# Kernel tuning notes

Hardware: AMD Instinct MI355X
Metric: run time of the kernel (lower is better)

Reference implementation:

```python
import jax, jax.numpy as jnp
import numpy as np

TOP_K = 2  # num_experts_per_token


def setup_inputs() -> dict:
    key = jax.random.key(0)
    k1, k2, k3, k4 = jax.random.split(key, 4)
    B, S, D, F, E = 2, 2048, 1024, 4096, 8
    hidden_states = jax.random.normal(k1, (B, S, D), dtype=jnp.float32)
    # router: nn.Linear(D, E, bias=False) -> weight [E, D]
    Wr = jax.random.normal(k2, (E, D), dtype=jnp.float32) * (1.0 / np.sqrt(D))
    # expert FFNs: W1 [E, D, F] (first Linear, transposed), W2 [E, F, D]
    W1 = jax.random.normal(k3, (E, D, F), dtype=jnp.float32) * (1.0 / np.sqrt(D))
    W2 = jax.random.normal(k4, (E, F, D), dtype=jnp.float32) * (1.0 / np.sqrt(F))
    return {"hidden_states": hidden_states, "Wr": Wr, "W1": W1, "W2": W2}


def reference(hidden_states, Wr, W1, W2):
    B, S, D = hidden_states.shape
    E = Wr.shape[0]
    x = hidden_states.reshape(-1, D)                      # [T, D]
    T = x.shape[0]

    router_logits = x @ Wr.T                              # [T, E]
    routing_weights = jax.nn.softmax(router_logits, axis=-1)
    top_w, top_idx = jax.lax.top_k(routing_weights, TOP_K)  # [T, K]
    top_w = top_w / jnp.sum(top_w, axis=-1, keepdims=True)

    # combine weights scattered into dense [T, E] (zero for unselected experts)
    comb = jnp.zeros((T, E), dtype=x.dtype).at[
        jnp.arange(T)[:, None], top_idx
    ].add(top_w)

    # per-expert FFN: SiLU(x @ W1) @ W2, computed densely then masked-combined
    h = jax.nn.silu(jnp.einsum('td,edf->tef', x, W1))     # [T, E, F]
    y = jnp.einsum('tef,efd->ted', h, W2)                 # [T, E, D]
    out = jnp.einsum('te,ted->td', comb, y)               # [T, D]
    return out.reshape(B, S, D)
```

## Files before the change

### kernel.cpp

```cpp
#include <hip/hip_runtime.h>
#include <hip/hip_bf16.h>

#define T_TOK 4096
#define DDIM  1024
#define FDIM  4096
#define NEXP  8
#define TLMAX 136

typedef __attribute__((ext_vector_type(8))) short bf16x8;
typedef __attribute__((ext_vector_type(4))) float f32x4;

__device__ __forceinline__ void gl2lds16(const void* g, void* l) {
  __builtin_amdgcn_global_load_lds((const __attribute__((address_space(1))) void*)g,
                                   (__attribute__((address_space(3))) void*)l,
                                   16, 0, 0);
}

__device__ __forceinline__ unsigned short f2bf(float f) {
  unsigned u = __float_as_uint(f);
  unsigned r = (u + 0x7fffu + ((u >> 16) & 1u)) >> 16;
  return (unsigned short)r;
}
__device__ __forceinline__ float bf2f(unsigned short u) {
  return __uint_as_float((unsigned)u << 16);
}

__global__ __launch_bounds__(256) void moe_router(
    const float* __restrict__ x, const float* __restrict__ Wr,
    unsigned short* __restrict__ xb, int* __restrict__ te, float* __restrict__ tw) {
  __shared__ float wr[NEXP * DDIM];
  const int tid = threadIdx.x;
#pragma unroll
  for (int i = 0; i < NEXP * DDIM / 256; ++i) wr[i * 256 + tid] = Wr[i * 256 + tid];
  __syncthreads();

  const int wave = tid >> 6, lane = tid & 63;
  const int t = blockIdx.x * 4 + wave;
  const float* xr = x + (size_t)t * DDIM;
  const int d0 = lane * 16;

  float4 xv[4];
#pragma unroll
  for (int j = 0; j < 4; ++j) xv[j] = *(const float4*)(xr + d0 + j * 4);

  float lg[NEXP];
#pragma unroll
  for (int e = 0; e < NEXP; ++e) {
    float s = 0.f;
#pragma unroll
    for (int j = 0; j < 4; ++j) {
      float4 wv = *(const float4*)(&wr[e * DDIM + d0 + j * 4]);
      s += xv[j].x * wv.x + xv[j].y * wv.y + xv[j].z * wv.z + xv[j].w * wv.w;
    }
    lg[e] = s;
  }
#pragma unroll
  for (int e = 0; e < NEXP; ++e) {
#pragma unroll
    for (int off = 32; off > 0; off >>= 1) lg[e] += __shfl_xor(lg[e], off);
  }

#pragma unroll
  for (int j = 0; j < 4; ++j) {
    ushort4 o;
    o.x = f2bf(xv[j].x); o.y = f2bf(xv[j].y); o.z = f2bf(xv[j].z); o.w = f2bf(xv[j].w);
    *(ushort4*)(xb + (size_t)t * DDIM + d0 + j * 4) = o;
  }

  if (lane == 0) {
    int i0 = 0;
#pragma unroll
    for (int e = 1; e < NEXP; ++e) if (lg[e] > lg[i0]) i0 = e;
    int i1 = (i0 == 0) ? 1 : 0;
#pragma unroll
    for (int e = 0; e < NEXP; ++e) if (e != i0 && lg[e] > lg[i1]) i1 = e;
    float w0 = 1.f / (1.f + __expf(lg[i1] - lg[i0]));
    te[t * 2 + 0] = i0; te[t * 2 + 1] = i1;
    tw[t * 2 + 0] = w0; tw[t * 2 + 1] = 1.f - w0;
  }
}

__global__ __launch_bounds__(256) void moe_count(const int* __restrict__ te,
                                                 int* __restrict__ counts) {
  __shared__ int lh[NEXP];
  const int tid = threadIdx.x;
  if (tid < NEXP) lh[tid] = 0;
  __syncthreads();
  const int t = blockIdx.x * 256 + tid;
  atomicAdd(&lh[te[t * 2 + 0]], 1);
  atomicAdd(&lh[te[t * 2 + 1]], 1);
  __syncthreads();
  if (tid < NEXP) atomicAdd(&counts[tid], lh[tid]);
}

__global__ void moe_prefix(const int* __restrict__ counts, int* __restrict__ offs,
                           int* __restrict__ fill, int* __restrict__ tcnt,
                           int* __restrict__ tlist) {
  if (threadIdx.x == 0) {
    int s = 0, tt = 0;
    for (int e = 0; e < NEXP; ++e) {
      offs[e] = s;
      int c = counts[e];
      s += c;
      fill[e] = 0;
      for (int mt = 0; mt * 64 < c; ++mt) tlist[tt++] = (e << 8) | mt;
    }
    offs[NEXP] = s;
    tcnt[0] = tt;
  }
}

__global__ __launch_bounds__(256) void moe_scatter(
    const int* __restrict__ te, const int* __restrict__ offs, int* __restrict__ fill,
    int* __restrict__ rows, int* __restrict__ slot) {
  __shared__ int lcnt[NEXP], lbase[NEXP];
  const int tid = threadIdx.x;
  if (tid < NEXP) lcnt[tid] = 0;
  __syncthreads();
  const int t = blockIdx.x * 256 + tid;
  const int e0 = te[t * 2 + 0], e1 = te[t * 2 + 1];
  const int r0 = atomicAdd(&lcnt[e0], 1);
  const int r1 = atomicAdd(&lcnt[e1], 1);
  __syncthreads();
  if (tid < NEXP) lbase[tid] = atomicAdd(&fill[tid], lcnt[tid]);
  __syncthreads();
  int p0 = offs[e0] + lbase[e0] + r0;
  int p1 = offs[e1] + lbase[e1] + r1;
  rows[p0] = t; rows[p1] = t;
  slot[t * 2 + 0] = p0; slot[t * 2 + 1] = p1;
}

__global__ __launch_bounds__(256) void wconv_t(const float* __restrict__ W,
                                               unsigned short* __restrict__ Wt,
                                               int K, int N) {
  __shared__ unsigned short t[64][65];
  const int e = blockIdx.z;
  const float* src = W + (size_t)e * K * N + (size_t)(blockIdx.y * 64) * N + blockIdx.x * 64;
  unsigned short* dst = Wt + (size_t)e * N * K + (size_t)(blockIdx.x * 64) * K + blockIdx.y * 64;
  const int tid = threadIdx.x;
  const int rr = tid >> 4;
  const int cc4 = (tid & 15) * 4;
#pragma unroll
  for (int i = 0; i < 4; ++i) {
    int r = i * 16 + rr;
    float4 v = *(const float4*)(src + (size_t)r * N + cc4);
    t[cc4 + 0][r] = f2bf(v.x);
    t[cc4 + 1][r] = f2bf(v.y);
    t[cc4 + 2][r] = f2bf(v.z);
    t[cc4 + 3][r] = f2bf(v.w);
  }
  __syncthreads();
  const int k8 = (tid & 7) * 8;
#pragma unroll
  for (int i = 0; i < 2; ++i) {
    int c = i * 32 + (tid >> 3);
    uint4 pk;
    pk.x = (unsigned)t[c][k8 + 0] | ((unsigned)t[c][k8 + 1] << 16);
    pk.y = (unsigned)t[c][k8 + 2] | ((unsigned)t[c][k8 + 3] << 16);
    pk.z = (unsigned)t[c][k8 + 4] | ((unsigned)t[c][k8 + 5] << 16);
    pk.w = (unsigned)t[c][k8 + 6] | ((unsigned)t[c][k8 + 7] << 16);
    *(uint4*)(dst + (size_t)c * K + k8) = pk;
  }
}

template <int KD, int KSLICE, int ND, bool GATHER, bool DOSILU>
__global__ __launch_bounds__(512, 4) void moe_gemm(
    const unsigned short* __restrict__ Asrc, const unsigned short* __restrict__ Wt,
    const int* __restrict__ rows, const int* __restrict__ offs,
    const int* __restrict__ tcnt, const int* __restrict__ tlist,
    unsigned short* __restrict__ Out) {
  constexpr int BM = 64, BN = 256;
  constexpr int S = KD / KSLICE;
  constexpr int NTN = ND / BN;
  constexpr int NPAN = NTN * S;
  constexpr int NB = TLMAX * NPAN;
  constexpr int CB = BN / 64;
  constexpr int MF = BM / 32, NF = 4;

  __shared__ alignas(16) unsigned short Alds[2][BM * 64];
  __shared__ alignas(16) unsigned short Blds[2][BN * 64];

  const int bid = blockIdx.x;
  const int orig = (bid & 7) * (NB >> 3) + (bid >> 3);
  const int TT = tcnt[0];
  if (orig >= TT * NPAN) return;
  const int tt = orig % TT;
  const int panel = orig / TT;
  const int nt = panel % NTN;
  const int ksl = panel / NTN;
  const int pk = tlist[tt];
  const int e = pk >> 8, mt = pk & 255;

  const int base = offs[e];
  const int cnt = offs[e + 1] - base;
  const int m0 = mt * BM;
  const int valid = min(BM, cnt - m0);
  const size_t koff = (size_t)ksl * KSLICE;

  const int tid = threadIdx.x;
  const int w = tid >> 6, lane = tid & 63;
  const int wm = w >> 2, wn = w & 3;

  const int n0 = nt * BN;
  const unsigned short* Wb = Wt + (size_t)e * ND * KD + (size_t)n0 * KD + koff;

  const int cc8 = ((lane & 7) ^ (lane >> 3)) * 8;
  const int ar = w * 8 + (lane >> 3);
  const int aslot = base + m0 + min(ar, valid - 1);
  const size_t aoff = (size_t)(GATHER ? rows[aslot] : aslot) * KD + koff + cc8;
  size_t boff[CB];
#pragma unroll
  for (int s = 0; s < CB; ++s) {
    int r = s * 64 + w * 8 + (lane >> 3);
    boff[s] = (size_t)r * KD + cc8;
  }

  f32x4 acc[MF][NF] = {};

#define STAGE(b, k0)                                                         \
  {                                                                          \
    gl2lds16(Asrc + aoff + (k0), &Alds[b][w * 512]);                         \
    _Pragma("unroll") for (int s = 0; s < CB; ++s)                           \
        gl2lds16(Wb + boff[s] + (k0), &Blds[b][(s * 512 + w * 64) * 8]);     \
  }

#define COMPUTE(b)                                                           \
  {                                                                          \
    _Pragma("unroll") for (int ks = 0; ks < 2; ++ks) {                       \
      bf16x8 af[MF], bfr[NF];                                                \
      _Pragma("unroll") for (int mf = 0; mf < MF; ++mf) {                    \
        int row = wm * 32 + mf * 16 + (lane & 15);                           \
        int cc = ks * 4 + (lane >> 4);                                       \
        af[mf] = *(const bf16x8*)((const char*)&Alds[b][0] + row * 128 +     \
                                  ((cc ^ (row & 7)) * 16));                  \
      }                                                                      \
      _Pragma("unroll") for (int nf = 0; nf < NF; ++nf) {                    \
        int col = wn * 64 + nf * 16 + (lane & 15);                           \
        int cc = ks * 4 + (lane >> 4);                                       \
        bfr[nf] = *(const bf16x8*)((const char*)&Blds[b][0] + col * 128 +    \
                                   ((cc ^ (col & 7)) * 16));                 \
      }                                                                      \
      _Pragma("unroll") for (int mf = 0; mf < MF; ++mf)                      \
          _Pragma("unroll") for (int nf = 0; nf < NF; ++nf)                  \
              acc[mf][nf] = __builtin_amdgcn_mfma_f32_16x16x32_bf16(         \
                  af[mf], bfr[nf], acc[mf][nf], 0, 0, 0);                    \
    }                                                                        \
  }

  constexpr int NK = KSLICE / 64;
  STAGE(0, 0);
  for (int t = 0; t < NK; t += 2) {
    STAGE(1, (t + 1) * 64);
    asm volatile("s_waitcnt vmcnt(5)" ::: "memory");
    __builtin_amdgcn_s_barrier();
    COMPUTE(0);
    __builtin_amdgcn_s_barrier();
    if (t + 2 < NK) {
      STAGE(0, (t + 2) * 64);
      asm volatile("s_waitcnt vmcnt(5)" ::: "memory");
    } else {
      asm volatile("s_waitcnt vmcnt(0)" ::: "memory");
    }
    __builtin_amdgcn_s_barrier();
    COMPUTE(1);
    __builtin_amdgcn_s_barrier();
  }
#undef STAGE
#undef COMPUTE

  unsigned short* Op = Out + (size_t)ksl * 8192 * ND;
  const int q = lane >> 4, c16 = lane & 15;
#pragma unroll
  for (int mf = 0; mf < MF; ++mf) {
#pragma unroll
    for (int r = 0; r < 4; ++r) {
      int lrow = wm * 32 + mf * 16 + q * 4 + r;
      if (lrow < valid) {
#pragma unroll
        for (int nf = 0; nf < NF; ++nf) {
          int gcol = n0 + wn * 64 + nf * 16 + c16;
          float v = acc[mf][nf][r];
          if (DOSILU) v = v / (1.f + __expf(-v));
          Op[(size_t)(base + m0 + lrow) * ND + gcol] = f2bf(v);
        }
      }
    }
  }
}

__global__ __launch_bounds__(256) void moe_combine(
    const unsigned short* __restrict__ y, const int* __restrict__ slot,
    const float* __restrict__ tw, float* __restrict__ out) {
  const int t = blockIdx.x;
  const int s0 = slot[t * 2], s1 = slot[t * 2 + 1];
  const float w0 = tw[t * 2], w1 = tw[t * 2 + 1];
  const int i = threadIdx.x * 4;
  ushort4 a = *(const ushort4*)(y + (size_t)s0 * DDIM + i);
  ushort4 b = *(const ushort4*)(y + (size_t)(8192 + s0) * DDIM + i);
  ushort4 c = *(const ushort4*)(y + (size_t)s1 * DDIM + i);
  ushort4 d = *(const ushort4*)(y + (size_t)(8192 + s1) * DDIM + i);
  float4 r;
  r.x = w0 * (bf2f(a.x) + bf2f(b.x)) + w1 * (bf2f(c.x) + bf2f(d.x));
  r.y = w0 * (bf2f(a.y) + bf2f(b.y)) + w1 * (bf2f(c.y) + bf2f(d.y));
  r.z = w0 * (bf2f(a.z) + bf2f(b.z)) + w1 * (bf2f(c.z) + bf2f(d.z));
  r.w = w0 * (bf2f(a.w) + bf2f(b.w)) + w1 * (bf2f(c.w) + bf2f(d.w));
  *(float4*)(out + (size_t)t * DDIM + i) = r;
}

extern "C" void kernel_launch(void* const* d_in, const int* in_sizes, int n_in,
                              void* d_out, int out_size, void* d_ws, size_t ws_size,
                              hipStream_t stream) {
  const float* x  = (const float*)d_in[0];
  const float* Wr = (const float*)d_in[1];
  const float* W1 = (const float*)d_in[2];
  const float* W2 = (const float*)d_in[3];
  float* out = (float*)d_out;

  char* ws = (char*)d_ws;
  unsigned short* xb = (unsigned short*)ws;
  unsigned short* H  = (unsigned short*)(ws + (size_t)(8 << 20));
  unsigned short* WT = (unsigned short*)(ws + (size_t)(72 << 20));
  unsigned short* y  = (unsigned short*)(ws + (size_t)(136 << 20));
  char* meta = ws + (size_t)(168 << 20);
  int* rows   = (int*)meta;
  int* te     = (int*)(meta + (32 << 10));
  float* tw   = (float*)(meta + (64 << 10));
  int* slot   = (int*)(meta + (96 << 10));
  int* counts = (int*)(meta + (128 << 10));
  int* offs   = counts + 16;
  int* fill   = counts + 32;
  int* tcnt   = counts + 48;
  int* tlist  = counts + 64;

  hipMemsetAsync(counts, 0, 256, stream);

  moe_router<<<T_TOK / 4, 256, 0, stream>>>(x, Wr, xb, te, tw);
  moe_count<<<T_TOK / 256, 256, 0, stream>>>(te, counts);
  moe_prefix<<<1, 64, 0, stream>>>(counts, offs, fill, tcnt, tlist);
  moe_scatter<<<T_TOK / 256, 256, 0, stream>>>(te, offs, fill, rows, slot);

  wconv_t<<<dim3(FDIM / 64, DDIM / 64, NEXP), 256, 0, stream>>>(W1, WT, DDIM, FDIM);
  moe_gemm<DDIM, DDIM, FDIM, true, true>
      <<<TLMAX * (FDIM / 256), 512, 0, stream>>>(xb, WT, rows, offs, tcnt, tlist, H);

  wconv_t<<<dim3(DDIM / 64, FDIM / 64, NEXP), 256, 0, stream>>>(W2, WT, FDIM, DDIM);
  moe_gemm<FDIM, FDIM / 2, DDIM, false, false>
      <<<TLMAX * (DDIM / 256) * 2, 512, 0, stream>>>(H, WT, nullptr, offs, tcnt, tlist, y);

  moe_combine<<<T_TOK, 256, 0, stream>>>(y, slot, tw, out);
}
```

Measured before the change: 310.8 us.

## Fuse weight conversion kernels into router and first GEMM launches

The W1 transpose/bf16 conversion now runs as extra blocks of the router kernel, and the W2 conversion runs as extra blocks of the first expert GEMM, each using separate WT1/WT2 buffers. This removes two standalone launches and lets the conversion work overlap with router and GEMM1 blocks, hiding tail and launch gaps. The cost is a larger workspace and GEMM1 blocks competing for bandwidth and CU slots with the conversion blocks.

```diff
diff --git a/kernel.cpp b/kernel.cpp
--- a/kernel.cpp
+++ b/kernel.cpp
@@ -25,17 +25,53 @@
   return __uint_as_float((unsigned)u << 16);
 }
 
-__global__ __launch_bounds__(256) void moe_router(
+__global__ __launch_bounds__(256) void moe_router_wc1(
     const float* __restrict__ x, const float* __restrict__ Wr,
+    const float* __restrict__ W1, unsigned short* __restrict__ WT1,
     unsigned short* __restrict__ xb, int* __restrict__ te, float* __restrict__ tw) {
   __shared__ float wr[NEXP * DDIM];
+  const int bid = blockIdx.x;
   const int tid = threadIdx.x;
+
+  if (bid >= T_TOK / 4) {
+    const int tau = bid - T_TOK / 4;
+    const int bx = tau & 63;
+    const int by = (tau >> 6) & 15;
+    const int e = tau >> 10;
+    unsigned short(*t)[65] = (unsigned short(*)[65])wr;
+    const float* src = W1 + (size_t)e * DDIM * FDIM + (size_t)(by * 64) * FDIM + bx * 64;
+    unsigned short* dst = WT1 + (size_t)e * FDIM * DDIM + (size_t)(bx * 64) * DDIM + by * 64;
+    const int rr = tid >> 4, cc4 = (tid & 15) * 4;
+#pragma unroll
+    for (int i = 0; i < 4; ++i) {
+      int r = i * 16 + rr;
+      float4 v = *(const float4*)(src + (size_t)r * FDIM + cc4);
+      t[cc4 + 0][r] = f2bf(v.x);
+      t[cc4 + 1][r] = f2bf(v.y);
+      t[cc4 + 2][r] = f2bf(v.z);
+      t[cc4 + 3][r] = f2bf(v.w);
+    }
+    __syncthreads();
+    const int k8 = (tid & 7) * 8;
+#pragma unroll
+    for (int i = 0; i < 2; ++i) {
+      int c = i * 32 + (tid >> 3);
+      uint4 pk;
+      pk.x = (unsigned)t[c][k8 + 0] | ((unsigned)t[c][k8 + 1] << 16);
+      pk.y = (unsigned)t[c][k8 + 2] | ((unsigned)t[c][k8 + 3] << 16);
+      pk.z = (unsigned)t[c][k8 + 4] | ((unsigned)t[c][k8 + 5] << 16);
+      pk.w = (unsigned)t[c][k8 + 6] | ((unsigned)t[c][k8 + 7] << 16);
+      *(uint4*)(dst + (size_t)c * DDIM + k8) = pk;
+    }
+    return;
+  }
+
 #pragma unroll
   for (int i = 0; i < NEXP * DDIM / 256; ++i) wr[i * 256 + tid] = Wr[i * 256 + tid];
   __syncthreads();
 
   const int wave = tid >> 6, lane = tid & 63;
-  const int t = blockIdx.x * 4 + wave;
+  const int t = bid * 4 + wave;
   const float* xr = x + (size_t)t * DDIM;
   const int d0 = lane * 16;
 
@@ -130,64 +166,63 @@
   slot[t * 2 + 0] = p0; slot[t * 2 + 1] = p1;
 }
 
-__global__ __launch_bounds__(256) void wconv_t(const float* __restrict__ W,
-                                               unsigned short* __restrict__ Wt,
-                                               int K, int N) {
-  __shared__ unsigned short t[64][65];
-  const int e = blockIdx.z;
-  const float* src = W + (size_t)e * K * N + (size_t)(blockIdx.y * 64) * N + blockIdx.x * 64;
-  unsigned short* dst = Wt + (size_t)e * N * K + (size_t)(blockIdx.x * 64) * K + blockIdx.y * 64;
-  const int tid = threadIdx.x;
-  const int rr = tid >> 4;
-  const int cc4 = (tid & 15) * 4;
-#pragma unroll
-  for (int i = 0; i < 4; ++i) {
-    int r = i * 16 + rr;
-    float4 v = *(const float4*)(src + (size_t)r * N + cc4);
-    t[cc4 + 0][r] = f2bf(v.x);
-    t[cc4 + 1][r] = f2bf(v.y);
-    t[cc4 + 2][r] = f2bf(v.z);
-    t[cc4 + 3][r] = f2bf(v.w);
-  }
-  __syncthreads();
-  const int k8 = (tid & 7) * 8;
-#pragma unroll
-  for (int i = 0; i < 2; ++i) {
-    int c = i * 32 + (tid >> 3);
-    uint4 pk;
-    pk.x = (unsigned)t[c][k8 + 0] | ((unsigned)t[c][k8 + 1] << 16);
-    pk.y = (unsigned)t[c][k8 + 2] | ((unsigned)t[c][k8 + 3] << 16);
-    pk.z = (unsigned)t[c][k8 + 4] | ((unsigned)t[c][k8 + 5] << 16);
-    pk.w = (unsigned)t[c][k8 + 6] | ((unsigned)t[c][k8 + 7] << 16);
-    *(uint4*)(dst + (size_t)c * K + k8) = pk;
-  }
-}
-
-template <int KD, int KSLICE, int ND, bool GATHER, bool DOSILU>
-__global__ __launch_bounds__(512, 4) void moe_gemm(
-    const unsigned short* __restrict__ Asrc, const unsigned short* __restrict__ Wt,
+__global__ __launch_bounds__(512, 4) void moe_gemm1_wc2(
+    const unsigned short* __restrict__ Asrc, const unsigned short* __restrict__ Wt1,
+    const float* __restrict__ W2, unsigned short* __restrict__ WT2,
     const int* __restrict__ rows, const int* __restrict__ offs,
     const int* __restrict__ tcnt, const int* __restrict__ tlist,
-    unsigned short* __restrict__ Out) {
-  constexpr int BM = 64, BN = 256;
-  constexpr int S = KD / KSLICE;
+    unsigned short* __restrict__ Hout) {
+  constexpr int KD = DDIM, ND = FDIM, BM = 64, BN = 256;
   constexpr int NTN = ND / BN;
-  constexpr int NPAN = NTN * S;
-  constexpr int NB = TLMAX * NPAN;
-  constexpr int CB = BN / 64;
-  constexpr int MF = BM / 32, NF = 4;
+  constexpr int NB = TLMAX * NTN;
+  constexpr int CB = BN / 64, MF = BM / 32, NF = 4;
 
   __shared__ alignas(16) unsigned short Alds[2][BM * 64];
   __shared__ alignas(16) unsigned short Blds[2][BN * 64];
 
   const int bid = blockIdx.x;
+  const int tid = threadIdx.x;
+
+  if (bid >= NB) {
+    const int wid = bid - NB;
+    const int sub = tid >> 8, t2 = tid & 255;
+    const int tau = wid * 2 + sub;
+    const int bx = tau & 15;
+    const int by = (tau >> 4) & 63;
+    const int e = tau >> 10;
+    unsigned short(*t)[65] = (unsigned short(*)[65])((char*)&Blds[0][0] + sub * 8320);
+    const float* src = W2 + (size_t)e * FDIM * DDIM + (size_t)(by * 64) * DDIM + bx * 64;
+    unsigned short* dst = WT2 + (size_t)e * DDIM * FDIM + (size_t)(bx * 64) * FDIM + by * 64;
+    const int rr = t2 >> 4, cc4 = (t2 & 15) * 4;
+#pragma unroll
+    for (int i = 0; i < 4; ++i) {
+      int r = i * 16 + rr;
+      float4 v = *(const float4*)(src + (size_t)r * DDIM + cc4);
+      t[cc4 + 0][r] = f2bf(v.x);
+      t[cc4 + 1][r] = f2bf(v.y);
+      t[cc4 + 2][r] = f2bf(v.z);
+      t[cc4 + 3][r] = f2bf(v.w);
+    }
+    __syncthreads();
+    const int k8 = (t2 & 7) * 8;
+#pragma unroll
+    for (int i = 0; i < 2; ++i) {
+      int c = i * 32 + (t2 >> 3);
+      uint4 pk;
+      pk.x = (unsigned)t[c][k8 + 0] | ((unsigned)t[c][k8 + 1] << 16);
+      pk.y = (unsigned)t[c][k8 + 2] | ((unsigned)t[c][k8 + 3] << 16);
+      pk.z = (unsigned)t[c][k8 + 4] | ((unsigned)t[c][k8 + 5] << 16);
+      pk.w = (unsigned)t[c][k8 + 6] | ((unsigned)t[c][k8 + 7] << 16);
+      *(uint4*)(dst + (size_t)c * FDIM + k8) = pk;
+    }
+    return;
+  }
+
   const int orig = (bid & 7) * (NB >> 3) + (bid >> 3);
   const int TT = tcnt[0];
-  if (orig >= TT * NPAN) return;
+  if (orig >= TT * NTN) return;
   const int tt = orig % TT;
-  const int panel = orig / TT;
-  const int nt = panel % NTN;
-  const int ksl = panel / NTN;
+  const int nt = orig / TT;
   const int pk = tlist[tt];
   const int e = pk >> 8, mt = pk & 255;
 
@@ -195,19 +230,17 @@
   const int cnt = offs[e + 1] - base;
   const int m0 = mt * BM;
   const int valid = min(BM, cnt - m0);
-  const size_t koff = (size_t)ksl * KSLICE;
-
-  const int tid = threadIdx.x;
+
   const int w = tid >> 6, lane = tid & 63;
   const int wm = w >> 2, wn = w & 3;
 
   const int n0 = nt * BN;
-  const unsigned short* Wb = Wt + (size_t)e * ND * KD + (size_t)n0 * KD + koff;
+  const unsigned short* Wb = Wt1 + (size_t)e * ND * KD + (size_t)n0 * KD;
 
   const int cc8 = ((lane & 7) ^ (lane >> 3)) * 8;
   const int ar = w * 8 + (lane >> 3);
   const int aslot = base + m0 + min(ar, valid - 1);
-  const size_t aoff = (size_t)(GATHER ? rows[aslot] : aslot) * KD + koff + cc8;
+  const size_t aoff = (size_t)rows[aslot] * KD + cc8;
   size_t boff[CB];
 #pragma unroll
   for (int s = 0; s < CB; ++s) {
@@ -247,6 +280,130 @@
     }                                                                        \
   }
 
+  constexpr int NK = KD / 64;
+  STAGE(0, 0);
+  for (int t = 0; t < NK; t += 2) {
+    STAGE(1, (t + 1) * 64);
+    asm volatile("s_waitcnt vmcnt(5)" ::: "memory");
+    __builtin_amdgcn_s_barrier();
+    COMPUTE(0);
+    __builtin_amdgcn_s_barrier();
+    if (t + 2 < NK) {
+      STAGE(0, (t + 2) * 64);
+      asm volatile("s_waitcnt vmcnt(5)" ::: "memory");
+    } else {
+      asm volatile("s_waitcnt vmcnt(0)" ::: "memory");
+    }
+    __builtin_amdgcn_s_barrier();
+    COMPUTE(1);
+    __builtin_amdgcn_s_barrier();
+  }
+#undef STAGE
+#undef COMPUTE
+
+  const int q = lane >> 4, c16 = lane & 15;
+#pragma unroll
+  for (int mf = 0; mf < MF; ++mf) {
+#pragma unroll
+    for (int r = 0; r < 4; ++r) {
+      int lrow = wm * 32 + mf * 16 + q * 4 + r;
+      if (lrow < valid) {
+#pragma unroll
+        for (int nf = 0; nf < NF; ++nf) {
+          int gcol = n0 + wn * 64 + nf * 16 + c16;
+          float v = acc[mf][nf][r];
+          v = v / (1.f + __expf(-v));
+          Hout[(size_t)(base + m0 + lrow) * ND + gcol] = f2bf(v);
+        }
+      }
+    }
+  }
+}
+
+template <int KD, int KSLICE, int ND, bool GATHER, bool DOSILU>
+__global__ __launch_bounds__(512, 4) void moe_gemm(
+    const unsigned short* __restrict__ Asrc, const unsigned short* __restrict__ Wt,
+    const int* __restrict__ rows, const int* __restrict__ offs,
+    const int* __restrict__ tcnt, const int* __restrict__ tlist,
+    unsigned short* __restrict__ Out) {
+  constexpr int BM = 64, BN = 256;
+  constexpr int S = KD / KSLICE;
+  constexpr int NTN = ND / BN;
+  constexpr int NPAN = NTN * S;
+  constexpr int NB = TLMAX * NPAN;
+  constexpr int CB = BN / 64;
+  constexpr int MF = BM / 32, NF = 4;
+
+  __shared__ alignas(16) unsigned short Alds[2][BM * 64];
+  __shared__ alignas(16) unsigned short Blds[2][BN * 64];
+
+  const int bid = blockIdx.x;
+  const int orig = (bid & 7) * (NB >> 3) + (bid >> 3);
+  const int TT = tcnt[0];
+  if (orig >= TT * NPAN) return;
+  const int tt = orig % TT;
+  const int panel = orig / TT;
+  const int nt = panel % NTN;
+  const int ksl = panel / NTN;
+  const int pk = tlist[tt];
+  const int e = pk >> 8, mt = pk & 255;
+
+  const int base = offs[e];
+  const int cnt = offs[e + 1] - base;
+  const int m0 = mt * BM;
+  const int valid = min(BM, cnt - m0);
+  const size_t koff = (size_t)ksl * KSLICE;
+
+  const int tid = threadIdx.x;
+  const int w = tid >> 6, lane = tid & 63;
+  const int wm = w >> 2, wn = w & 3;
+
+  const int n0 = nt * BN;
+  const unsigned short* Wb = Wt + (size_t)e * ND * KD + (size_t)n0 * KD + koff;
+
+  const int cc8 = ((lane & 7) ^ (lane >> 3)) * 8;
+  const int ar = w * 8 + (lane >> 3);
+  const int aslot = base + m0 + min(ar, valid - 1);
+  const size_t aoff = (size_t)(GATHER ? rows[aslot] : aslot) * KD + koff + cc8;
+  size_t boff[CB];
+#pragma unroll
+  for (int s = 0; s < CB; ++s) {
+    int r = s * 64 + w * 8 + (lane >> 3);
+    boff[s] = (size_t)r * KD + cc8;
+  }
+
+  f32x4 acc[MF][NF] = {};
+
+#define STAGE(b, k0)                                                         \
+  {                                                                          \
+    gl2lds16(Asrc + aoff + (k0), &Alds[b][w * 512]);                         \
+    _Pragma("unroll") for (int s = 0; s < CB; ++s)                           \
+        gl2lds16(Wb + boff[s] + (k0), &Blds[b][(s * 512 + w * 64) * 8]);     \
+  }
+
+#define COMPUTE(b)                                                           \
+  {                                                                          \
+    _Pragma("unroll") for (int ks = 0; ks < 2; ++ks) {                       \
+      bf16x8 af[MF], bfr[NF];                                                \
+      _Pragma("unroll") for (int mf = 0; mf < MF; ++mf) {                    \
+        int row = wm * 32 + mf * 16 + (lane & 15);                           \
+        int cc = ks * 4 + (lane >> 4);                                       \
+        af[mf] = *(const bf16x8*)((const char*)&Alds[b][0] + row * 128 +     \
+                                  ((cc ^ (row & 7)) * 16));                  \
+      }                                                                      \
+      _Pragma("unroll") for (int nf = 0; nf < NF; ++nf) {                    \
+        int col = wn * 64 + nf * 16 + (lane & 15);                           \
+        int cc = ks * 4 + (lane >> 4);                                       \
+        bfr[nf] = *(const bf16x8*)((const char*)&Blds[b][0] + col * 128 +    \
+                                   ((cc ^ (col & 7)) * 16));                 \
+      }                                                                      \
+      _Pragma("unroll") for (int mf = 0; mf < MF; ++mf)                      \
+          _Pragma("unroll") for (int nf = 0; nf < NF; ++nf)                  \
+              acc[mf][nf] = __builtin_amdgcn_mfma_f32_16x16x32_bf16(         \
+                  af[mf], bfr[nf], acc[mf][nf], 0, 0, 0);                    \
+    }                                                                        \
+  }
+
   constexpr int NK = KSLICE / 64;
   STAGE(0, 0);
   for (int t = 0; t < NK; t += 2) {
@@ -317,11 +474,12 @@
   float* out = (float*)d_out;
 
   char* ws = (char*)d_ws;
-  unsigned short* xb = (unsigned short*)ws;
-  unsigned short* H  = (unsigned short*)(ws + (size_t)(8 << 20));
-  unsigned short* WT = (unsigned short*)(ws + (size_t)(72 << 20));
-  unsigned short* y  = (unsigned short*)(ws + (size_t)(136 << 20));
-  char* meta = ws + (size_t)(168 << 20);
+  unsigned short* xb  = (unsigned short*)ws;
+  unsigned short* H   = (unsigned short*)(ws + (size_t)(8 << 20));
+  unsigned short* WT1 = (unsigned short*)(ws + (size_t)(72 << 20));
+  unsigned short* WT2 = (unsigned short*)(ws + (size_t)(136 << 20));
+  unsigned short* y   = (unsigned short*)(ws + (size_t)(200 << 20));
+  char* meta = ws + (size_t)(232 << 20);
   int* rows   = (int*)meta;
   int* te     = (int*)(meta + (32 << 10));
   float* tw   = (float*)(meta + (64 << 10));
@@ -334,18 +492,16 @@
 
   hipMemsetAsync(counts, 0, 256, stream);
 
-  moe_router<<<T_TOK / 4, 256, 0, stream>>>(x, Wr, xb, te, tw);
+  moe_router_wc1<<<T_TOK / 4 + 8192, 256, 0, stream>>>(x, Wr, W1, WT1, xb, te, tw);
   moe_count<<<T_TOK / 256, 256, 0, stream>>>(te, counts);
   moe_prefix<<<1, 64, 0, stream>>>(counts, offs, fill, tcnt, tlist);
   moe_scatter<<<T_TOK / 256, 256, 0, stream>>>(te, offs, fill, rows, slot);
 
-  wconv_t<<<dim3(FDIM / 64, DDIM / 64, NEXP), 256, 0, stream>>>(W1, WT, DDIM, FDIM);
-  moe_gemm<DDIM, DDIM, FDIM, true, true>
-      <<<TLMAX * (FDIM / 256), 512, 0, stream>>>(xb, WT, rows, offs, tcnt, tlist, H);
-
-  wconv_t<<<dim3(DDIM / 64, FDIM / 64, NEXP), 256, 0, stream>>>(W2, WT, FDIM, DDIM);
+  moe_gemm1_wc2<<<TLMAX * (FDIM / 256) + 4096, 512, 0, stream>>>(
+      xb, WT1, W2, WT2, rows, offs, tcnt, tlist, H);
+
   moe_gemm<FDIM, FDIM / 2, DDIM, false, false>
-      <<<TLMAX * (DDIM / 256) * 2, 512, 0, stream>>>(H, WT, nullptr, offs, tcnt, tlist, y);
+      <<<TLMAX * (DDIM / 256) * 2, 512, 0, stream>>>(H, WT2, nullptr, offs, tcnt, tlist, y);
 
   moe_combine<<<T_TOK, 256, 0, stream>>>(y, slot, tw, out);
 }
```

Measured after the change: 307.1 us (median of 2 runs). About the same (-1.2%).
